# Optimization experiments

Hardware: AMD Instinct MI355X
Metric: run time of the kernel (lower is better)

The kernel has to match this reference:

```python
import jax, jax.numpy as jnp
from jax import lax
import numpy as np

B, T, D, H, LAT, FUT = 2048, 64, 64, 256, 64, 96
NL = 10  # LSTM layers


def _lstm_layer(x, Wih, Whh, b):
    # x: [B, T, Din]; Wih: [4H, Din]; Whh: [4H, H]; b: [4H]
    xg = jnp.einsum('btd,gd->tbg', x, Wih) + b  # precompute input projections [T,B,4H]
    h0 = jnp.zeros((x.shape[0], Whh.shape[1]), x.dtype)

    def step(carry, xt):
        h, c = carry
        g = xt + h @ Whh.T
        i, f, gg, o = jnp.split(g, 4, axis=-1)  # torch gate order i,f,g,o
        c = jax.nn.sigmoid(f) * c + jax.nn.sigmoid(i) * jnp.tanh(gg)
        h = jax.nn.sigmoid(o) * jnp.tanh(c)
        return (h, c), h

    _, hs = lax.scan(step, (h0, h0), xg)
    return jnp.transpose(hs, (1, 0, 2))  # [B,T,H]


def setup_inputs() -> dict:
    key = jax.random.key(0)
    ks = iter(jax.random.split(key, 40))
    s = 0.05
    n = lambda shape: jax.random.normal(next(ks), shape, jnp.float32) * s
    inp = {
        'X': jax.random.normal(next(ks), (B, T, D), jnp.float32),
        'Wih0': n((4 * H, D)),
        'Wih': n((NL - 1, 4 * H, H)),
        'Whh': n((NL, 4 * H, H)),
        'b': n((NL, 4 * H)),  # b_ih + b_hh folded together
        'ef1w': n((128, H)), 'ef1b': n((128,)),
        'ef2w': n((64, 128)), 'ef2b': n((64,)),
        'mean_w': n((LAT, 64)), 'mean_b': n((LAT,)),
        'logvar_w': n((LAT, 64)), 'logvar_b': n((LAT,)),
        'scale_w': n((LAT, 64)), 'scale_b': n((LAT,)),
        'shape_w': n((LAT, 64)), 'shape_b': n((LAT,)),
        'df1w': n((128, LAT)), 'df1b': n((128,)),
        'df2w': n((500, 128)), 'df2b': n((500,)),
        'outw': n((FUT, 500)), 'outb': n((FUT,)),
        'finw': n((FUT, FUT)), 'finb': n((FUT,)),
        'pi_gaussian': jnp.asarray(0.9, jnp.float32),
        'eps': jax.random.normal(next(ks), (B, LAT), jnp.float32),
        'u': jax.random.uniform(next(ks), (B, LAT), jnp.float32),
        'choice': jax.random.uniform(next(ks), (B,), jnp.float32),
    }
    return inp


def reference(X, Wih0, Wih, Whh, b, ef1w, ef1b, ef2w, ef2b,
              mean_w, mean_b, logvar_w, logvar_b, scale_w, scale_b,
              shape_w, shape_b, df1w, df1b, df2w, df2b, outw, outb,
              finw, finb, pi_gaussian, eps, u, choice):
    # ---- Encoder: 10-layer LSTM, last hidden state ----
    h = _lstm_layer(X, Wih0, Whh[0], b[0])
    for l in range(1, NL):
        h = _lstm_layer(h, Wih[l - 1], Whh[l], b[l])
    last = h[:, -1, :]  # [B,H]
    hid = jax.nn.relu(last @ ef1w.T + ef1b)
    hid = jax.nn.relu(hid @ ef2w.T + ef2b)  # dropout = identity (eval)
    z_mean = hid @ mean_w.T + mean_b
    z_logvar = hid @ logvar_w.T + logvar_b
    z_scale = jnp.exp(hid @ scale_w.T + scale_b)
    z_shape = hid @ shape_w.T + shape_b
    # ---- Reparameterize: vectorized gaussian/GPD row selection ----
    z_gauss = z_mean + eps * jnp.exp(0.5 * z_logvar)
    z_gpd = z_scale / z_shape * (jnp.exp(-z_shape * jnp.log1p(-u)) - 1.0)
    z = jnp.where(choice[:, None] < pi_gaussian, z_gauss, z_gpd)
    # ---- Decoder ----
    d = jax.nn.relu(z @ df1w.T + df1b)
    d = jax.nn.relu(d @ df2w.T + df2b)
    out = d @ outw.T + outb
    final = out @ finw.T + finb
    return (final, z_mean, z_logvar, z_scale, z_shape)
```

## Files before the change

### kernel.cpp

```cpp
#include <hip/hip_runtime.h>

typedef unsigned short u16;
typedef unsigned int   u32;
typedef _Float16 v8hf __attribute__((ext_vector_type(8)));
typedef float  f32x4 __attribute__((ext_vector_type(4)));

static constexpr int B_   = 2048;
static constexpr int T_   = 64;
static constexpr int D_   = 64;
static constexpr int H_   = 256;
static constexpr int NL_  = 10;
static constexpr int FUT_ = 96;
static constexpr int NBLK = 128;

static constexpr size_t WF_LAYER_ELEMS = 524288;
static constexpr size_t SEQ_OFF        = 16u << 20;

__device__ __forceinline__ u16 f2h(float f) {
  _Float16 h = (_Float16)f;
  return __builtin_bit_cast(u16, h);
}
__device__ __forceinline__ float h2f(u16 b) {
  return (float)__builtin_bit_cast(_Float16, b);
}
__device__ __forceinline__ float rcp_(float x) { return __builtin_amdgcn_rcpf(x); }
__device__ __forceinline__ float fsig(float x) { return rcp_(1.f + __expf(-x)); }
__device__ __forceinline__ float ftanh(float x) {
  float e = __expf(-2.f * fabsf(x));
  float t = (1.f - e) * rcp_(1.f + e);
  return copysignf(t, x);
}

__device__ __forceinline__ void gld16(const u16* g, u16* l) {
  __builtin_amdgcn_global_load_lds(
      (const __attribute__((address_space(1))) void*)g,
      (__attribute__((address_space(3))) void*)l,
      16, 0, 0);
}

__global__ void pack_weights_v8(const float* __restrict__ Wih0,
                                const float* __restrict__ Wih,
                                const float* __restrict__ Whh,
                                u16* __restrict__ wf) {
  int gid = blockIdx.x * 256 + threadIdx.x;
  int l   = gid >> 16;
  if (l >= NL_) return;
  int rem  = gid & 65535;
  int kc   = rem >> 12;
  int cg   = (rem >> 8) & 15;
  int g    = (rem >> 6) & 3;
  int lane = rem & 63;
  const int NKC = (l == 0) ? 10 : 16;
  if (kc >= NKC) return;
  const int KX = (l == 0) ? 64 : 256;

  int row = g * 256 + cg * 16 + (lane & 15);
  int k0  = kc * 32 + (lane >> 4) * 8;

  float v[8];
#pragma unroll
  for (int i = 0; i < 8; ++i) {
    int k = k0 + i;
    float x;
    if (l == 0) x = (k < KX) ? Wih0[row * 64 + k] : Whh[row * 256 + (k - KX)];
    else        x = (k < KX) ? Wih[(size_t)((l - 1) * 1024 + row) * 256 + k]
                             : Whh[(size_t)(l * 1024 + row) * 256 + (k - KX)];
    v[i] = x;
  }
  u32 pk[4];
#pragma unroll
  for (int i = 0; i < 4; ++i)
    pk[i] = (u32)f2h(v[2 * i]) | ((u32)f2h(v[2 * i + 1]) << 16);
  uint4 val; val.x = pk[0]; val.y = pk[1]; val.z = pk[2]; val.w = pk[3];
  u16* dst = wf + (size_t)l * WF_LAYER_ELEMS
                + ((size_t)(kc * 16 + cg) * 4 + g) * 512 + (size_t)lane * 8;
  *(uint4*)dst = val;
}

template <int NKC, int KX, bool L0>
__global__ __launch_bounds__(1024, 4) void lstm_layer_v8(
    const float* __restrict__ X,
    u16* __restrict__ seq,
    const u16* __restrict__ wf,
    const float* __restrict__ bias)
{
  __shared__ __align__(16) u16 Albs[16 * 512];
  __shared__ __align__(16) u16 Wbuf[2][32768];

  const int tid  = threadIdx.x;
  const int wid  = tid >> 6;
  const int lane = tid & 63;
  const int bid  = blockIdx.x;
  const int arow = lane & 15;
  const int ahi  = lane >> 4;
  const int aswz = (arow & 7) << 4;
  const int j    = wid * 16 + arow;

  {
    int r = tid >> 6, o = (tid & 63) * 16;
    uint4 z; z.x = z.y = z.z = z.w = 0;
    *(uint4*)((char*)Albs + r * 1024 + o) = z;
  }

  float c[4] = {0.f, 0.f, 0.f, 0.f};
  float bv[4];
#pragma unroll
  for (int g = 0; g < 4; ++g) bv[g] = bias[g * 256 + j];

  const u16* wsrc = wf + (size_t)wid * 2048 + (size_t)lane * 8;
  u16* wdst0 = &Wbuf[0][wid * 2048];
  u16* wdst1 = &Wbuf[1][wid * 2048];

#pragma unroll
  for (int g = 0; g < 4; ++g) gld16(wsrc + g * 512, wdst0 + g * 512);

  for (int t = 0; t < T_; ++t) {
    if constexpr (L0) {
      int r = tid >> 6, k = tid & 63;
      float xv = X[((size_t)(bid * 16 + r) * T_ + t) * D_ + k];
      *(u16*)((char*)Albs + r * 1024 + ((k * 2) ^ ((r & 7) << 4))) = f2h(xv);
    } else {
      int r = tid >> 6, seg = tid & 63;
      uint2 v = *(const uint2*)(seq + ((((size_t)bid * T_ + t) * 16 + r) << 8) + seg * 4);
      *(uint2*)((char*)Albs + r * 1024 + ((seg * 8) ^ ((r & 7) << 4))) = v;
    }
    __syncthreads();

    f32x4 acc[4];
#pragma unroll
    for (int g = 0; g < 4; ++g) {
      acc[g][0] = bv[g]; acc[g][1] = bv[g]; acc[g][2] = bv[g]; acc[g][3] = bv[g];
    }

#pragma unroll
    for (int kc = 0; kc < NKC; ++kc) {
      if (kc + 1 < NKC) {
        u16* nd = ((kc + 1) & 1) ? wdst1 : wdst0;
#pragma unroll
        for (int g = 0; g < 4; ++g)
          gld16(wsrc + (size_t)(kc + 1) * 32768 + g * 512, nd + g * 512);
        asm volatile("s_waitcnt vmcnt(4)" ::: "memory");
      } else {
        asm volatile("s_waitcnt vmcnt(0)" ::: "memory");
      }
      __builtin_amdgcn_sched_barrier(0);

      v8hf a = *(const v8hf*)((const char*)Albs + arow * 1024 +
                              ((kc * 64 + ahi * 16) ^ aswz));
      const u16* wl = ((kc & 1) ? wdst1 : wdst0) + lane * 8;
#pragma unroll
      for (int g = 0; g < 4; ++g) {
        v8hf bw = *(const v8hf*)(const void*)(wl + g * 512);
        acc[g] = __builtin_amdgcn_mfma_f32_16x16x32_f16(a, bw, acc[g], 0, 0, 0);
      }
    }
    __syncthreads();

    __builtin_amdgcn_sched_barrier(0);
#pragma unroll
    for (int g = 0; g < 4; ++g) gld16(wsrc + g * 512, wdst0 + g * 512);

    u16* sbase = seq + ((((size_t)bid * T_ + t) * 16) << 8) + j;
#pragma unroll
    for (int q = 0; q < 4; ++q) {
      int r = ahi * 4 + q;
      float cn = fsig(acc[1][q]) * c[q] + fsig(acc[0][q]) * ftanh(acc[2][q]);
      c[q] = cn;
      float h = fsig(acc[3][q]) * ftanh(cn);
      u16 hb = f2h(h);
      sbase[(size_t)r << 8] = hb;
      *(u16*)((char*)Albs + r * 1024 + (((KX + j) * 2) ^ ((r & 7) << 4))) = hb;
    }
  }
}

template <int N, int K, bool RELU>
__device__ __forceinline__ void dense(const float (*__restrict__ in)[512],
                                      float (*__restrict__ out)[512],
                                      const float* __restrict__ W,
                                      const float* __restrict__ bg, int tid) {
  for (int e = tid; e < 16 * N; e += 256) {
    int r = e / N, n = e - r * N;
    const float* wr = W + (size_t)n * K;
    const float* ar = in[r];
    float4 acc = {0.f, 0.f, 0.f, 0.f};
    for (int k = 0; k < K; k += 4) {
      float4 wv = *(const float4*)(wr + k);
      float4 av = *(const float4*)(ar + k);
      acc.x = fmaf(wv.x, av.x, acc.x);
      acc.y = fmaf(wv.y, av.y, acc.y);
      acc.z = fmaf(wv.z, av.z, acc.z);
      acc.w = fmaf(wv.w, av.w, acc.w);
    }
    float s = bg[n] + acc.x + acc.y + acc.z + acc.w;
    out[r][n] = RELU ? fmaxf(s, 0.f) : s;
  }
}

template <int K>
__device__ __forceinline__ float dotK(const float* __restrict__ a, const float* __restrict__ w) {
  float4 acc = {0.f, 0.f, 0.f, 0.f};
#pragma unroll
  for (int k = 0; k < K; k += 4) {
    float4 wv = *(const float4*)(w + k);
    float4 av = *(const float4*)(a + k);
    acc.x = fmaf(wv.x, av.x, acc.x);
    acc.y = fmaf(wv.y, av.y, acc.y);
    acc.z = fmaf(wv.z, av.z, acc.z);
    acc.w = fmaf(wv.w, av.w, acc.w);
  }
  return acc.x + acc.y + acc.z + acc.w;
}

struct TailArgs {
  const u16* seq;
  const float *ef1w, *ef1b, *ef2w, *ef2b;
  const float *mean_w, *mean_b, *logvar_w, *logvar_b;
  const float *scale_w, *scale_b, *shape_w, *shape_b;
  const float *df1w, *df1b, *df2w, *df2b, *outw, *outb, *finw, *finb;
  const float *pi, *eps, *u, *choice;
  float* out;
};

__global__ __launch_bounds__(256) void tail_kernel_v8(TailArgs A) {
  __shared__ float a0[16][512];
  __shared__ float a1[16][512];
  const int tid = threadIdx.x, bid = blockIdx.x;

  for (int e = tid; e < 16 * 256; e += 256) {
    int r = e >> 8, jj = e & 255;
    a0[r][jj] = h2f(A.seq[((((size_t)bid * T_ + (T_ - 1)) * 16 + r) << 8) + jj]);
  }
  __syncthreads();

  dense<128, 256, true>(a0, a1, A.ef1w, A.ef1b, tid); __syncthreads();
  dense<64, 128, true>(a1, a0, A.ef2w, A.ef2b, tid);  __syncthreads();

  const float pi = *A.pi;
  for (int e = tid; e < 16 * 64; e += 256) {
    int r = e >> 6, n = e & 63;
    size_t rg = (size_t)bid * 16 + r;
    float m  = dotK<64>(a0[r], A.mean_w   + n * 64) + A.mean_b[n];
    float lv = dotK<64>(a0[r], A.logvar_w + n * 64) + A.logvar_b[n];
    float sc = __expf(dotK<64>(a0[r], A.scale_w + n * 64) + A.scale_b[n]);
    float sh = dotK<64>(a0[r], A.shape_w + n * 64) + A.shape_b[n];
    A.out[196608 + rg * 64 + n] = m;
    A.out[327680 + rg * 64 + n] = lv;
    A.out[458752 + rg * 64 + n] = sc;
    A.out[589824 + rg * 64 + n] = sh;
    float zg = m + A.eps[rg * 64 + n] * __expf(0.5f * lv);
    float L  = log1pf(-A.u[rg * 64 + n]);
    float zp = sc / sh * (__expf(-sh * L) - 1.f);
    a1[r][n] = (A.choice[rg] < pi) ? zg : zp;
  }
  __syncthreads();

  dense<128, 64, true>(a1, a0, A.df1w, A.df1b, tid);   __syncthreads();
  dense<500, 128, true>(a0, a1, A.df2w, A.df2b, tid);  __syncthreads();
  dense<96, 500, false>(a1, a0, A.outw, A.outb, tid);  __syncthreads();
  dense<96, 96, false>(a0, a1, A.finw, A.finb, tid);   __syncthreads();

  for (int e = tid; e < 16 * FUT_; e += 256) {
    int r = e / FUT_, n = e - r * FUT_;
    A.out[((size_t)bid * 16 + r) * FUT_ + n] = a1[r][n];
  }
}

extern "C" void kernel_launch(void* const* d_in, const int* in_sizes, int n_in,
                              void* d_out, int out_size, void* d_ws, size_t ws_size,
                              hipStream_t stream) {
  (void)in_sizes; (void)n_in; (void)out_size; (void)ws_size;

  const float* X      = (const float*)d_in[0];
  const float* Wih0   = (const float*)d_in[1];
  const float* Wih    = (const float*)d_in[2];
  const float* Whh    = (const float*)d_in[3];
  const float* b      = (const float*)d_in[4];
  const float* ef1w   = (const float*)d_in[5];
  const float* ef1b   = (const float*)d_in[6];
  const float* ef2w   = (const float*)d_in[7];
  const float* ef2b   = (const float*)d_in[8];
  const float* mean_w = (const float*)d_in[9];
  const float* mean_b = (const float*)d_in[10];
  const float* logvar_w = (const float*)d_in[11];
  const float* logvar_b = (const float*)d_in[12];
  const float* scale_w  = (const float*)d_in[13];
  const float* scale_b  = (const float*)d_in[14];
  const float* shape_w  = (const float*)d_in[15];
  const float* shape_b  = (const float*)d_in[16];
  const float* df1w   = (const float*)d_in[17];
  const float* df1b   = (const float*)d_in[18];
  const float* df2w   = (const float*)d_in[19];
  const float* df2b   = (const float*)d_in[20];
  const float* outw   = (const float*)d_in[21];
  const float* outb   = (const float*)d_in[22];
  const float* finw   = (const float*)d_in[23];
  const float* finb   = (const float*)d_in[24];
  const float* pi_g   = (const float*)d_in[25];
  const float* eps    = (const float*)d_in[26];
  const float* u      = (const float*)d_in[27];
  const float* choice = (const float*)d_in[28];

  u16* wf  = (u16*)d_ws;
  u16* seq = (u16*)((char*)d_ws + SEQ_OFF);
  float* out = (float*)d_out;

  pack_weights_v8<<<2560, 256, 0, stream>>>(Wih0, Wih, Whh, wf);

  lstm_layer_v8<10, 64, true><<<NBLK, 1024, 0, stream>>>(X, seq, wf, b);
  for (int l = 1; l < NL_; ++l)
    lstm_layer_v8<16, 256, false><<<NBLK, 1024, 0, stream>>>(nullptr, seq,
        wf + (size_t)l * WF_LAYER_ELEMS, b + l * 1024);

  TailArgs A;
  A.seq = seq;
  A.ef1w = ef1w; A.ef1b = ef1b; A.ef2w = ef2w; A.ef2b = ef2b;
  A.mean_w = mean_w; A.mean_b = mean_b; A.logvar_w = logvar_w; A.logvar_b = logvar_b;
  A.scale_w = scale_w; A.scale_b = scale_b; A.shape_w = shape_w; A.shape_b = shape_b;
  A.df1w = df1w; A.df1b = df1b; A.df2w = df2w; A.df2b = df2b;
  A.outw = outw; A.outb = outb; A.finw = finw; A.finb = finb;
  A.pi = pi_g; A.eps = eps; A.u = u; A.choice = choice;
  A.out = out;
  tail_kernel_v8<<<NBLK, 256, 0, stream>>>(A);
}
```

Measured before the change: 12.58 ms.

## Precompute input projections in 4-step chunks, separating them from the recurrent matmul

```diff
diff --git a/kernel.cpp b/kernel.cpp
--- a/kernel.cpp
+++ b/kernel.cpp
@@ -16,6 +16,14 @@
 static constexpr size_t WF_LAYER_ELEMS = 524288;
 static constexpr size_t SEQ_OFF        = 16u << 20;
 
+static constexpr size_t WFH_OFF  = 0;
+static constexpr size_t WFX_OFF  = 5u << 20;
+static constexpr size_t XG_OFF   = 10u << 20;
+static constexpr size_t SEQ2_OFF = 26u << 20;
+static constexpr size_t WS_NEED_V9 = SEQ2_OFF + (64ull << 20);
+static constexpr int    WFL9 = 262144;
+static constexpr int    TCH  = 4;
+
 __device__ __forceinline__ u16 f2h(float f) {
   _Float16 h = (_Float16)f;
   return __builtin_bit_cast(u16, h);
@@ -30,7 +38,6 @@
   float t = (1.f - e) * rcp_(1.f + e);
   return copysignf(t, x);
 }
-
 __device__ __forceinline__ void gld16(const u16* g, u16* l) {
   __builtin_amdgcn_global_load_lds(
       (const __attribute__((address_space(1))) void*)g,
@@ -82,8 +89,7 @@
     const float* __restrict__ X,
     u16* __restrict__ seq,
     const u16* __restrict__ wf,
-    const float* __restrict__ bias)
-{
+    const float* __restrict__ bias) {
   __shared__ __align__(16) u16 Albs[16 * 512];
   __shared__ __align__(16) u16 Wbuf[2][32768];
 
@@ -170,6 +176,244 @@
       u16 hb = f2h(h);
       sbase[(size_t)r << 8] = hb;
       *(u16*)((char*)Albs + r * 1024 + (((KX + j) * 2) ^ ((r & 7) << 4))) = hb;
+    }
+  }
+}
+
+__global__ void pack_weights_v9(const float* __restrict__ Wih0,
+                                const float* __restrict__ Wih,
+                                const float* __restrict__ Whh,
+                                u16* __restrict__ wfh,
+                                u16* __restrict__ wfx) {
+  int gid = blockIdx.x * 256 + threadIdx.x;
+  int lw  = gid >> 15;
+  if (lw >= NL_ * 2) return;
+  int l = lw >> 1, which = lw & 1;
+  int rem  = gid & 32767;
+  int kc   = rem >> 12;
+  int cg   = (rem >> 8) & 15;
+  int g    = (rem >> 6) & 3;
+  int lane = rem & 63;
+  if (which == 1 && l == 0 && kc >= 2) return;
+
+  int row = g * 256 + cg * 16 + (lane & 15);
+  int k0  = kc * 32 + (lane >> 4) * 8;
+
+  float v[8];
+#pragma unroll
+  for (int i = 0; i < 8; ++i) {
+    int k = k0 + i;
+    float x;
+    if (which == 0)      x = Whh[(size_t)(l * 1024 + row) * 256 + k];
+    else if (l == 0)     x = Wih0[row * 64 + k];
+    else                 x = Wih[(size_t)((l - 1) * 1024 + row) * 256 + k];
+    v[i] = x;
+  }
+  u32 pk[4];
+#pragma unroll
+  for (int i = 0; i < 4; ++i)
+    pk[i] = (u32)f2h(v[2 * i]) | ((u32)f2h(v[2 * i + 1]) << 16);
+  uint4 val; val.x = pk[0]; val.y = pk[1]; val.z = pk[2]; val.w = pk[3];
+  u16* base = (which == 0) ? wfh : wfx;
+  u16* dst = base + (size_t)l * WFL9
+                  + ((size_t)(kc * 16 + cg) * 4 + g) * 512 + (size_t)lane * 8;
+  *(uint4*)dst = val;
+}
+
+template <bool L0>
+__global__ __launch_bounds__(1024, 4) void lstm_layer_v9(
+    const float* __restrict__ X,
+    u16* __restrict__ seq,
+    const u16* __restrict__ wfx_l,
+    const u16* __restrict__ wfh_l,
+    u16* __restrict__ xg,
+    const float* __restrict__ bias) {
+  __shared__ __align__(16) u16 Wbuf[2][32768];
+  __shared__ __align__(16) u16 Ah[16 * 256];
+
+  const int tid  = threadIdx.x;
+  const int wid  = tid >> 6;
+  const int lane = tid & 63;
+  const int bid  = blockIdx.x;
+  const int arow = lane & 15;
+  const int ahi  = lane >> 4;
+  const int j    = wid * 16 + arow;
+
+  *(uint2*)((char*)Ah + tid * 8) = make_uint2(0, 0);
+
+  float c[4] = {0.f, 0.f, 0.f, 0.f};
+  float bv[4];
+#pragma unroll
+  for (int g = 0; g < 4; ++g) bv[g] = bias[g * 256 + j];
+
+  u16* wdst0 = &Wbuf[0][wid * 2048];
+  u16* wdst1 = &Wbuf[1][wid * 2048];
+  const size_t laneoff = (size_t)lane * 8;
+  u16* xgb = xg + (size_t)bid * 65536;
+  uint2 xr[4];
+
+  __syncthreads();
+
+  for (int tc = 0; tc < T_ / TCH; ++tc) {
+    f32x4 acc0[TCH][4];
+#pragma unroll
+    for (int rf = 0; rf < TCH; ++rf)
+#pragma unroll
+      for (int g = 0; g < 4; ++g) {
+        acc0[rf][g][0] = bv[g]; acc0[rf][g][1] = bv[g];
+        acc0[rf][g][2] = bv[g]; acc0[rf][g][3] = bv[g];
+      }
+
+    if constexpr (L0) {
+#pragma unroll
+      for (int g = 0; g < 4; ++g) {
+        gld16(wfx_l + ((size_t)(0 * 16 + wid) * 4 + g) * 512 + laneoff, wdst0 + g * 512);
+        gld16(wfx_l + ((size_t)(1 * 16 + wid) * 4 + g) * 512 + laneoff, wdst1 + g * 512);
+      }
+      asm volatile("s_waitcnt vmcnt(0)" ::: "memory");
+      __builtin_amdgcn_sched_barrier(0);
+      const float* xb = X + ((size_t)(bid * 16 + arow) * T_ + tc * TCH) * D_ + ahi * 8;
+#pragma unroll
+      for (int kc = 0; kc < 2; ++kc) {
+        const u16* wl = (kc ? wdst1 : wdst0) + lane * 8;
+        v8hf af[TCH];
+#pragma unroll
+        for (int rf = 0; rf < TCH; ++rf) {
+          float4 u = *(const float4*)(xb + rf * D_ + kc * 32);
+          float4 v2 = *(const float4*)(xb + rf * D_ + kc * 32 + 4);
+          v8hf a;
+          a[0] = (_Float16)u.x;  a[1] = (_Float16)u.y;
+          a[2] = (_Float16)u.z;  a[3] = (_Float16)u.w;
+          a[4] = (_Float16)v2.x; a[5] = (_Float16)v2.y;
+          a[6] = (_Float16)v2.z; a[7] = (_Float16)v2.w;
+          af[rf] = a;
+        }
+#pragma unroll
+        for (int g = 0; g < 4; ++g) {
+          v8hf w = *(const v8hf*)(const void*)(wl + g * 512);
+#pragma unroll
+          for (int rf = 0; rf < TCH; ++rf)
+            acc0[rf][g] = __builtin_amdgcn_mfma_f32_16x16x32_f16(af[rf], w, acc0[rf][g], 0, 0, 0);
+        }
+      }
+    } else {
+      const u16* abase = seq + ((size_t)(bid * T_ + tc * TCH) * 16 + arow) * 256 + ahi * 8;
+      v8hf aA[TCH], aB[TCH];
+#pragma unroll
+      for (int g = 0; g < 4; ++g)
+        gld16(wfx_l + ((size_t)(0 * 16 + wid) * 4 + g) * 512 + laneoff, wdst0 + g * 512);
+#pragma unroll
+      for (int rf = 0; rf < TCH; ++rf)
+        aA[rf] = *(const v8hf*)(const void*)(abase + rf * 4096);
+
+#pragma unroll
+      for (int kc = 0; kc < 8; ++kc) {
+        if (kc < 7) {
+          u16* nd = ((kc + 1) & 1) ? wdst1 : wdst0;
+#pragma unroll
+          for (int g = 0; g < 4; ++g)
+            gld16(wfx_l + ((size_t)((kc + 1) * 16 + wid) * 4 + g) * 512 + laneoff, nd + g * 512);
+          if ((kc & 1) == 0) {
+#pragma unroll
+            for (int rf = 0; rf < TCH; ++rf)
+              aB[rf] = *(const v8hf*)(const void*)(abase + rf * 4096 + (kc + 1) * 32);
+          } else {
+#pragma unroll
+            for (int rf = 0; rf < TCH; ++rf)
+              aA[rf] = *(const v8hf*)(const void*)(abase + rf * 4096 + (kc + 1) * 32);
+          }
+          asm volatile("s_waitcnt vmcnt(8)" ::: "memory");
+        } else {
+          asm volatile("s_waitcnt vmcnt(0)" ::: "memory");
+        }
+        __builtin_amdgcn_sched_barrier(0);
+        const u16* wl = ((kc & 1) ? wdst1 : wdst0) + lane * 8;
+#pragma unroll
+        for (int g = 0; g < 4; ++g) {
+          v8hf w = *(const v8hf*)(const void*)(wl + g * 512);
+#pragma unroll
+          for (int rf = 0; rf < TCH; ++rf)
+            acc0[rf][g] = __builtin_amdgcn_mfma_f32_16x16x32_f16(
+                ((kc & 1) ? aB[rf] : aA[rf]), w, acc0[rf][g], 0, 0, 0);
+        }
+      }
+    }
+
+#pragma unroll
+    for (int rf = 0; rf < TCH; ++rf)
+#pragma unroll
+      for (int g = 0; g < 4; ++g) {
+        uint2 pk;
+        pk.x = (u32)f2h(acc0[rf][g][0]) | ((u32)f2h(acc0[rf][g][1]) << 16);
+        pk.y = (u32)f2h(acc0[rf][g][2]) | ((u32)f2h(acc0[rf][g][3]) << 16);
+        *(uint2*)(xgb + (((size_t)(rf * 1024 + g * 256 + j)) << 4) + ahi * 4) = pk;
+      }
+    __syncthreads();
+
+#pragma unroll
+    for (int g = 0; g < 4; ++g)
+      xr[g] = *(const uint2*)(xgb + (((size_t)(0 * 1024 + g * 256 + j)) << 4) + ahi * 4);
+#pragma unroll
+    for (int g = 0; g < 4; ++g)
+      gld16(wfh_l + ((size_t)(0 * 16 + wid) * 4 + g) * 512 + laneoff, wdst0 + g * 512);
+
+    for (int tl = 0; tl < TCH; ++tl) {
+      const int t = tc * TCH + tl;
+      f32x4 acc[4];
+#pragma unroll
+      for (int g = 0; g < 4; ++g) {
+        acc[g][0] = h2f((u16)(xr[g].x & 0xffff));
+        acc[g][1] = h2f((u16)(xr[g].x >> 16));
+        acc[g][2] = h2f((u16)(xr[g].y & 0xffff));
+        acc[g][3] = h2f((u16)(xr[g].y >> 16));
+      }
+
+#pragma unroll
+      for (int kc = 0; kc < 8; ++kc) {
+        if (kc < 7) {
+          u16* nd = ((kc + 1) & 1) ? wdst1 : wdst0;
+#pragma unroll
+          for (int g = 0; g < 4; ++g)
+            gld16(wfh_l + ((size_t)((kc + 1) * 16 + wid) * 4 + g) * 512 + laneoff, nd + g * 512);
+          asm volatile("s_waitcnt vmcnt(4)" ::: "memory");
+        } else {
+          asm volatile("s_waitcnt vmcnt(0)" ::: "memory");
+        }
+        __builtin_amdgcn_sched_barrier(0);
+
+        v8hf a = *(const v8hf*)((const char*)Ah + arow * 512 +
+                                ((kc * 64 + ahi * 16) ^ ((arow & 7) << 4)));
+        const u16* wl = ((kc & 1) ? wdst1 : wdst0) + lane * 8;
+#pragma unroll
+        for (int g = 0; g < 4; ++g) {
+          v8hf w = *(const v8hf*)(const void*)(wl + g * 512);
+          acc[g] = __builtin_amdgcn_mfma_f32_16x16x32_f16(a, w, acc[g], 0, 0, 0);
+        }
+      }
+      __syncthreads();
+
+      if (tl + 1 < TCH) {
+#pragma unroll
+        for (int g = 0; g < 4; ++g)
+          xr[g] = *(const uint2*)(xgb + (((size_t)((tl + 1) * 1024 + g * 256 + j)) << 4) + ahi * 4);
+        __builtin_amdgcn_sched_barrier(0);
+#pragma unroll
+        for (int g = 0; g < 4; ++g)
+          gld16(wfh_l + ((size_t)(0 * 16 + wid) * 4 + g) * 512 + laneoff, wdst0 + g * 512);
+      }
+
+      u16* sbase = seq + ((((size_t)bid * T_ + t) * 16) << 8) + j;
+#pragma unroll
+      for (int q = 0; q < 4; ++q) {
+        int r = ahi * 4 + q;
+        float cn = fsig(acc[1][q]) * c[q] + fsig(acc[0][q]) * ftanh(acc[2][q]);
+        c[q] = cn;
+        float h = fsig(acc[3][q]) * ftanh(cn);
+        u16 hb = f2h(h);
+        sbase[(size_t)r << 8] = hb;
+        *(u16*)((char*)Ah + r * 512 + ((j * 2) ^ ((r & 7) << 4))) = hb;
+      }
+      __syncthreads();
     }
   }
 }
@@ -269,7 +513,7 @@
 extern "C" void kernel_launch(void* const* d_in, const int* in_sizes, int n_in,
                               void* d_out, int out_size, void* d_ws, size_t ws_size,
                               hipStream_t stream) {
-  (void)in_sizes; (void)n_in; (void)out_size; (void)ws_size;
+  (void)in_sizes; (void)n_in; (void)out_size;
 
   const float* X      = (const float*)d_in[0];
   const float* Wih0   = (const float*)d_in[1];
@@ -301,16 +545,33 @@
   const float* u      = (const float*)d_in[27];
   const float* choice = (const float*)d_in[28];
 
-  u16* wf  = (u16*)d_ws;
-  u16* seq = (u16*)((char*)d_ws + SEQ_OFF);
   float* out = (float*)d_out;
-
-  pack_weights_v8<<<2560, 256, 0, stream>>>(Wih0, Wih, Whh, wf);
-
-  lstm_layer_v8<10, 64, true><<<NBLK, 1024, 0, stream>>>(X, seq, wf, b);
-  for (int l = 1; l < NL_; ++l)
-    lstm_layer_v8<16, 256, false><<<NBLK, 1024, 0, stream>>>(nullptr, seq,
-        wf + (size_t)l * WF_LAYER_ELEMS, b + l * 1024);
+  const bool big = ws_size >= WS_NEED_V9;
+  u16* seq;
+
+  if (big) {
+    u16* wfh = (u16*)((char*)d_ws + WFH_OFF);
+    u16* wfx = (u16*)((char*)d_ws + WFX_OFF);
+    u16* xg  = (u16*)((char*)d_ws + XG_OFF);
+    seq      = (u16*)((char*)d_ws + SEQ2_OFF);
+
+    pack_weights_v9<<<2560, 256, 0, stream>>>(Wih0, Wih, Whh, wfh, wfx);
+
+    lstm_layer_v9<true><<<NBLK, 1024, 0, stream>>>(X, seq, wfx, wfh, xg, b);
+    for (int l = 1; l < NL_; ++l)
+      lstm_layer_v9<false><<<NBLK, 1024, 0, stream>>>(nullptr, seq,
+          wfx + (size_t)l * WFL9, wfh + (size_t)l * WFL9, xg, b + l * 1024);
+  } else {
+    u16* wf = (u16*)d_ws;
+    seq     = (u16*)((char*)d_ws + SEQ_OFF);
+
+    pack_weights_v8<<<2560, 256, 0, stream>>>(Wih0, Wih, Whh, wf);
+
+    lstm_layer_v8<10, 64, true><<<NBLK, 1024, 0, stream>>>(X, seq, wf, b);
+    for (int l = 1; l < NL_; ++l)
+      lstm_layer_v8<16, 256, false><<<NBLK, 1024, 0, stream>>>(nullptr, seq,
+          wf + (size_t)l * WF_LAYER_ELEMS, b + l * 1024);
+  }
 
   TailArgs A;
   A.seq = seq;
```

After: 10.67 ms. -15.2%, faster.

## Split LSTM input projection from recurrence, batching x-gates over time chunks

Applied to the files above, without the earlier changes.

```diff
diff --git a/kernel.cpp b/kernel.cpp
--- a/kernel.cpp
+++ b/kernel.cpp
@@ -4,6 +4,7 @@
 typedef unsigned int   u32;
 typedef _Float16 v8hf __attribute__((ext_vector_type(8)));
 typedef float  f32x4 __attribute__((ext_vector_type(4)));
+typedef u32    u32x2 __attribute__((ext_vector_type(2)));
 
 static constexpr int B_   = 2048;
 static constexpr int T_   = 64;
@@ -13,8 +14,12 @@
 static constexpr int FUT_ = 96;
 static constexpr int NBLK = 128;
 
-static constexpr size_t WF_LAYER_ELEMS = 524288;
-static constexpr size_t SEQ_OFF        = 16u << 20;
+static constexpr size_t WFH_OFF  = 0;
+static constexpr size_t WFX_OFF  = 5u << 20;
+static constexpr size_t XG_OFF   = 10u << 20;
+static constexpr size_t SEQ2_OFF = 26u << 20;
+static constexpr int    WFL9 = 262144;
+static constexpr int    TCH  = 4;
 
 __device__ __forceinline__ u16 f2h(float f) {
   _Float16 h = (_Float16)f;
@@ -30,7 +35,6 @@
   float t = (1.f - e) * rcp_(1.f + e);
   return copysignf(t, x);
 }
-
 __device__ __forceinline__ void gld16(const u16* g, u16* l) {
   __builtin_amdgcn_global_load_lds(
       (const __attribute__((address_space(1))) void*)g,
@@ -38,21 +42,21 @@
       16, 0, 0);
 }
 
-__global__ void pack_weights_v8(const float* __restrict__ Wih0,
-                                const float* __restrict__ Wih,
-                                const float* __restrict__ Whh,
-                                u16* __restrict__ wf) {
+__global__ void pack_weights_v11(const float* __restrict__ Wih0,
+                                 const float* __restrict__ Wih,
+                                 const float* __restrict__ Whh,
+                                 u16* __restrict__ wfh,
+                                 u16* __restrict__ wfx) {
   int gid = blockIdx.x * 256 + threadIdx.x;
-  int l   = gid >> 16;
-  if (l >= NL_) return;
-  int rem  = gid & 65535;
+  int lw  = gid >> 15;
+  if (lw >= NL_ * 2) return;
+  int l = lw >> 1, which = lw & 1;
+  int rem  = gid & 32767;
   int kc   = rem >> 12;
   int cg   = (rem >> 8) & 15;
   int g    = (rem >> 6) & 3;
   int lane = rem & 63;
-  const int NKC = (l == 0) ? 10 : 16;
-  if (kc >= NKC) return;
-  const int KX = (l == 0) ? 64 : 256;
+  if (which == 1 && l == 0 && kc >= 2) return;
 
   int row = g * 256 + cg * 16 + (lane & 15);
   int k0  = kc * 32 + (lane >> 4) * 8;
@@ -62,9 +66,9 @@
   for (int i = 0; i < 8; ++i) {
     int k = k0 + i;
     float x;
-    if (l == 0) x = (k < KX) ? Wih0[row * 64 + k] : Whh[row * 256 + (k - KX)];
-    else        x = (k < KX) ? Wih[(size_t)((l - 1) * 1024 + row) * 256 + k]
-                             : Whh[(size_t)(l * 1024 + row) * 256 + (k - KX)];
+    if (which == 0)      x = Whh[(size_t)(l * 1024 + row) * 256 + k];
+    else if (l == 0)     x = Wih0[row * 64 + k];
+    else                 x = Wih[(size_t)((l - 1) * 1024 + row) * 256 + k];
     v[i] = x;
   }
   u32 pk[4];
@@ -72,20 +76,22 @@
   for (int i = 0; i < 4; ++i)
     pk[i] = (u32)f2h(v[2 * i]) | ((u32)f2h(v[2 * i + 1]) << 16);
   uint4 val; val.x = pk[0]; val.y = pk[1]; val.z = pk[2]; val.w = pk[3];
-  u16* dst = wf + (size_t)l * WF_LAYER_ELEMS
-                + ((size_t)(kc * 16 + cg) * 4 + g) * 512 + (size_t)lane * 8;
+  u16* base = (which == 0) ? wfh : wfx;
+  u16* dst = base + (size_t)l * WFL9
+                  + ((size_t)(kc * 16 + cg) * 4 + g) * 512 + (size_t)lane * 8;
   *(uint4*)dst = val;
 }
 
-template <int NKC, int KX, bool L0>
-__global__ __launch_bounds__(1024, 4) void lstm_layer_v8(
+template <bool L0>
+__global__ __launch_bounds__(1024, 4) void lstm_layer_v11(
     const float* __restrict__ X,
     u16* __restrict__ seq,
-    const u16* __restrict__ wf,
-    const float* __restrict__ bias)
-{
-  __shared__ __align__(16) u16 Albs[16 * 512];
-  __shared__ __align__(16) u16 Wbuf[2][32768];
+    const u16* __restrict__ wfx_l,
+    const u16* __restrict__ wfh_l,
+    u16* __restrict__ xg,
+    const float* __restrict__ bias) {
+  __shared__ __align__(16) u16 Wring[65536];
+  __shared__ __align__(16) u16 Ah[16 * 256];
 
   const int tid  = threadIdx.x;
   const int wid  = tid >> 6;
@@ -93,83 +99,196 @@
   const int bid  = blockIdx.x;
   const int arow = lane & 15;
   const int ahi  = lane >> 4;
-  const int aswz = (arow & 7) << 4;
   const int j    = wid * 16 + arow;
 
-  {
-    int r = tid >> 6, o = (tid & 63) * 16;
-    uint4 z; z.x = z.y = z.z = z.w = 0;
-    *(uint4*)((char*)Albs + r * 1024 + o) = z;
-  }
+  *(u32x2*)((char*)Ah + tid * 8) = (u32x2){0, 0};
 
   float c[4] = {0.f, 0.f, 0.f, 0.f};
   float bv[4];
 #pragma unroll
   for (int g = 0; g < 4; ++g) bv[g] = bias[g * 256 + j];
 
-  const u16* wsrc = wf + (size_t)wid * 2048 + (size_t)lane * 8;
-  u16* wdst0 = &Wbuf[0][wid * 2048];
-  u16* wdst1 = &Wbuf[1][wid * 2048];
-
-#pragma unroll
-  for (int g = 0; g < 4; ++g) gld16(wsrc + g * 512, wdst0 + g * 512);
-
-  for (int t = 0; t < T_; ++t) {
+  u16* wdst0 = Wring + wid * 2048;
+  u16* wdst1 = Wring + 32768 + wid * 2048;
+  const size_t laneoff = (size_t)lane * 8;
+  u16* xgb = xg + (size_t)bid * 65536;
+  u32x2 xr[4];
+
+  __syncthreads();
+
+  for (int tc = 0; tc < T_ / TCH; ++tc) {
+    f32x4 acc0[TCH][4];
+#pragma unroll
+    for (int rf = 0; rf < TCH; ++rf)
+#pragma unroll
+      for (int g = 0; g < 4; ++g) {
+        acc0[rf][g][0] = bv[g]; acc0[rf][g][1] = bv[g];
+        acc0[rf][g][2] = bv[g]; acc0[rf][g][3] = bv[g];
+      }
+
     if constexpr (L0) {
-      int r = tid >> 6, k = tid & 63;
-      float xv = X[((size_t)(bid * 16 + r) * T_ + t) * D_ + k];
-      *(u16*)((char*)Albs + r * 1024 + ((k * 2) ^ ((r & 7) << 4))) = f2h(xv);
+#pragma unroll
+      for (int g = 0; g < 4; ++g) {
+        gld16(wfx_l + ((size_t)(0 * 16 + wid) * 4 + g) * 512 + laneoff, wdst0 + g * 512);
+        gld16(wfx_l + ((size_t)(1 * 16 + wid) * 4 + g) * 512 + laneoff, wdst1 + g * 512);
+      }
+      asm volatile("s_waitcnt vmcnt(0)" ::: "memory");
+      __builtin_amdgcn_sched_barrier(0);
+      const float* xb = X + ((size_t)(bid * 16 + arow) * T_ + tc * TCH) * D_ + ahi * 8;
+#pragma unroll
+      for (int kc = 0; kc < 2; ++kc) {
+        const u16* wl = (kc ? wdst1 : wdst0) + lane * 8;
+        v8hf af[TCH];
+#pragma unroll
+        for (int rf = 0; rf < TCH; ++rf) {
+          f32x4 u = __builtin_nontemporal_load((const f32x4*)(xb + rf * D_ + kc * 32));
+          f32x4 v2 = __builtin_nontemporal_load((const f32x4*)(xb + rf * D_ + kc * 32 + 4));
+          v8hf a;
+          a[0] = (_Float16)u[0];  a[1] = (_Float16)u[1];
+          a[2] = (_Float16)u[2];  a[3] = (_Float16)u[3];
+          a[4] = (_Float16)v2[0]; a[5] = (_Float16)v2[1];
+          a[6] = (_Float16)v2[2]; a[7] = (_Float16)v2[3];
+          af[rf] = a;
+        }
+#pragma unroll
+        for (int g = 0; g < 4; ++g) {
+          v8hf w = *(const v8hf*)(const void*)(wl + g * 512);
+#pragma unroll
+          for (int rf = 0; rf < TCH; ++rf)
+            acc0[rf][g] = __builtin_amdgcn_mfma_f32_16x16x32_f16(af[rf], w, acc0[rf][g], 0, 0, 0);
+        }
+      }
     } else {
-      int r = tid >> 6, seg = tid & 63;
-      uint2 v = *(const uint2*)(seq + ((((size_t)bid * T_ + t) * 16 + r) << 8) + seg * 4);
-      *(uint2*)((char*)Albs + r * 1024 + ((seg * 8) ^ ((r & 7) << 4))) = v;
+      const u16* abase = seq + ((size_t)(bid * T_ + tc * TCH) * 16 + arow) * 256 + ahi * 8;
+      v8hf aA[TCH], aB[TCH];
+#pragma unroll
+      for (int g = 0; g < 4; ++g)
+        gld16(wfx_l + ((size_t)(0 * 16 + wid) * 4 + g) * 512 + laneoff, wdst0 + g * 512);
+#pragma unroll
+      for (int rf = 0; rf < TCH; ++rf)
+        aA[rf] = __builtin_nontemporal_load((const v8hf*)(const void*)(abase + rf * 4096));
+
+#pragma unroll
+      for (int kc = 0; kc < 8; ++kc) {
+        if (kc < 7) {
+          u16* nd = ((kc + 1) & 1) ? wdst1 : wdst0;
+#pragma unroll
+          for (int g = 0; g < 4; ++g)
+            gld16(wfx_l + ((size_t)((kc + 1) * 16 + wid) * 4 + g) * 512 + laneoff, nd + g * 512);
+          if ((kc & 1) == 0) {
+#pragma unroll
+            for (int rf = 0; rf < TCH; ++rf)
+              aB[rf] = __builtin_nontemporal_load(
+                  (const v8hf*)(const void*)(abase + rf * 4096 + (kc + 1) * 32));
+          } else {
+#pragma unroll
+            for (int rf = 0; rf < TCH; ++rf)
+              aA[rf] = __builtin_nontemporal_load(
+                  (const v8hf*)(const void*)(abase + rf * 4096 + (kc + 1) * 32));
+          }
+          asm volatile("s_waitcnt vmcnt(8)" ::: "memory");
+        } else {
+          asm volatile("s_waitcnt vmcnt(0)" ::: "memory");
+        }
+        __builtin_amdgcn_sched_barrier(0);
+        const u16* wl = ((kc & 1) ? wdst1 : wdst0) + lane * 8;
+#pragma unroll
+        for (int g = 0; g < 4; ++g) {
+          v8hf w = *(const v8hf*)(const void*)(wl + g * 512);
+#pragma unroll
+          for (int rf = 0; rf < TCH; ++rf)
+            acc0[rf][g] = __builtin_amdgcn_mfma_f32_16x16x32_f16(
+                ((kc & 1) ? aB[rf] : aA[rf]), w, acc0[rf][g], 0, 0, 0);
+        }
+      }
     }
+
+#pragma unroll
+    for (int rf = 0; rf < TCH; ++rf)
+#pragma unroll
+      for (int g = 0; g < 4; ++g) {
+        u32x2 pk;
+        pk[0] = (u32)f2h(acc0[rf][g][0]) | ((u32)f2h(acc0[rf][g][1]) << 16);
+        pk[1] = (u32)f2h(acc0[rf][g][2]) | ((u32)f2h(acc0[rf][g][3]) << 16);
+        __builtin_nontemporal_store(pk,
+            (u32x2*)(xgb + (((size_t)(rf * 1024 + g * 256 + j)) << 4) + ahi * 4));
+      }
     __syncthreads();
 
-    f32x4 acc[4];
-#pragma unroll
-    for (int g = 0; g < 4; ++g) {
-      acc[g][0] = bv[g]; acc[g][1] = bv[g]; acc[g][2] = bv[g]; acc[g][3] = bv[g];
-    }
-
-#pragma unroll
-    for (int kc = 0; kc < NKC; ++kc) {
-      if (kc + 1 < NKC) {
-        u16* nd = ((kc + 1) & 1) ? wdst1 : wdst0;
+#pragma unroll
+    for (int g = 0; g < 4; ++g)
+      xr[g] = __builtin_nontemporal_load(
+          (const u32x2*)(xgb + (((size_t)(0 * 1024 + g * 256 + j)) << 4) + ahi * 4));
+
+    for (int tl = 0; tl < TCH; ++tl) {
+      const int t = tc * TCH + tl;
+      f32x4 acc[4];
+#pragma unroll
+      for (int g = 0; g < 4; ++g) {
+        acc[g][0] = h2f((u16)(xr[g][0] & 0xffff));
+        acc[g][1] = h2f((u16)(xr[g][0] >> 16));
+        acc[g][2] = h2f((u16)(xr[g][1] & 0xffff));
+        acc[g][3] = h2f((u16)(xr[g][1] >> 16));
+      }
+
+#pragma unroll
+      for (int u0 = 0; u0 < 3; ++u0) {
+        const int kc = u0 >> 1, gh = u0 & 1;
+        u16* sb = Wring + (u0 & 3) * 16384 + wid * 1024;
+#pragma unroll
+        for (int jj = 0; jj < 2; ++jj)
+          gld16(wfh_l + ((size_t)(kc * 16 + wid) * 4 + gh * 2 + jj) * 512 + laneoff,
+                sb + jj * 512);
+      }
+
+      v8hf a{};
+#pragma unroll
+      for (int u = 0; u < 16; ++u) {
+        const int kc = u >> 1, gh = u & 1;
+        if (u + 3 <= 15) {
+          const int un = u + 3, kn = un >> 1, gn = un & 1;
+          u16* sb = Wring + (un & 3) * 16384 + wid * 1024;
+#pragma unroll
+          for (int jj = 0; jj < 2; ++jj)
+            gld16(wfh_l + ((size_t)(kn * 16 + wid) * 4 + gn * 2 + jj) * 512 + laneoff,
+                  sb + jj * 512);
+        }
+        if (u <= 12)      asm volatile("s_waitcnt vmcnt(6)" ::: "memory");
+        else if (u == 13) asm volatile("s_waitcnt vmcnt(4)" ::: "memory");
+        else if (u == 14) asm volatile("s_waitcnt vmcnt(2)" ::: "memory");
+        else              asm volatile("s_waitcnt vmcnt(0)" ::: "memory");
+        __builtin_amdgcn_sched_barrier(0);
+
+        if (gh == 0)
+          a = *(const v8hf*)((const char*)Ah + arow * 512 +
+                             ((kc * 64 + ahi * 16) ^ ((arow & 7) << 4)));
+        const u16* wl = Wring + (u & 3) * 16384 + wid * 1024 + lane * 8;
+        v8hf w0 = *(const v8hf*)(const void*)(wl);
+        v8hf w1 = *(const v8hf*)(const void*)(wl + 512);
+        acc[gh * 2]     = __builtin_amdgcn_mfma_f32_16x16x32_f16(a, w0, acc[gh * 2], 0, 0, 0);
+        acc[gh * 2 + 1] = __builtin_amdgcn_mfma_f32_16x16x32_f16(a, w1, acc[gh * 2 + 1], 0, 0, 0);
+      }
+      __syncthreads();
+
+      if (tl + 1 < TCH) {
 #pragma unroll
         for (int g = 0; g < 4; ++g)
-          gld16(wsrc + (size_t)(kc + 1) * 32768 + g * 512, nd + g * 512);
-        asm volatile("s_waitcnt vmcnt(4)" ::: "memory");
-      } else {
-        asm volatile("s_waitcnt vmcnt(0)" ::: "memory");
-      }
-      __builtin_amdgcn_sched_barrier(0);
-
-      v8hf a = *(const v8hf*)((const char*)Albs + arow * 1024 +
-                              ((kc * 64 + ahi * 16) ^ aswz));
-      const u16* wl = ((kc & 1) ? wdst1 : wdst0) + lane * 8;
-#pragma unroll
-      for (int g = 0; g < 4; ++g) {
-        v8hf bw = *(const v8hf*)(const void*)(wl + g * 512);
-        acc[g] = __builtin_amdgcn_mfma_f32_16x16x32_f16(a, bw, acc[g], 0, 0, 0);
-      }
-    }
-    __syncthreads();
-
-    __builtin_amdgcn_sched_barrier(0);
-#pragma unroll
-    for (int g = 0; g < 4; ++g) gld16(wsrc + g * 512, wdst0 + g * 512);
-
-    u16* sbase = seq + ((((size_t)bid * T_ + t) * 16) << 8) + j;
-#pragma unroll
-    for (int q = 0; q < 4; ++q) {
-      int r = ahi * 4 + q;
-      float cn = fsig(acc[1][q]) * c[q] + fsig(acc[0][q]) * ftanh(acc[2][q]);
-      c[q] = cn;
-      float h = fsig(acc[3][q]) * ftanh(cn);
-      u16 hb = f2h(h);
-      sbase[(size_t)r << 8] = hb;
-      *(u16*)((char*)Albs + r * 1024 + (((KX + j) * 2) ^ ((r & 7) << 4))) = hb;
+          xr[g] = __builtin_nontemporal_load(
+              (const u32x2*)(xgb + (((size_t)((tl + 1) * 1024 + g * 256 + j)) << 4) + ahi * 4));
+      }
+
+      u16* sbase = seq + ((((size_t)bid * T_ + t) * 16) << 8) + j;
+#pragma unroll
+      for (int q = 0; q < 4; ++q) {
+        int r = ahi * 4 + q;
+        float cn = fsig(acc[1][q]) * c[q] + fsig(acc[0][q]) * ftanh(acc[2][q]);
+        c[q] = cn;
+        float h = fsig(acc[3][q]) * ftanh(cn);
+        u16 hb = f2h(h);
+        __builtin_nontemporal_store(hb, sbase + ((size_t)r << 8));
+        *(u16*)((char*)Ah + r * 512 + ((j * 2) ^ ((r & 7) << 4))) = hb;
+      }
+      __syncthreads();
     }
   }
 }
@@ -222,7 +341,7 @@
   float* out;
 };
 
-__global__ __launch_bounds__(256) void tail_kernel_v8(TailArgs A) {
+__global__ __launch_bounds__(256) void tail_kernel_v11(TailArgs A) {
   __shared__ float a0[16][512];
   __shared__ float a1[16][512];
   const int tid = threadIdx.x, bid = blockIdx.x;
@@ -301,16 +420,18 @@
   const float* u      = (const float*)d_in[27];
   const float* choice = (const float*)d_in[28];
 
-  u16* wf  = (u16*)d_ws;
-  u16* seq = (u16*)((char*)d_ws + SEQ_OFF);
   float* out = (float*)d_out;
-
-  pack_weights_v8<<<2560, 256, 0, stream>>>(Wih0, Wih, Whh, wf);
-
-  lstm_layer_v8<10, 64, true><<<NBLK, 1024, 0, stream>>>(X, seq, wf, b);
+  u16* wfh = (u16*)((char*)d_ws + WFH_OFF);
+  u16* wfx = (u16*)((char*)d_ws + WFX_OFF);
+  u16* xg  = (u16*)((char*)d_ws + XG_OFF);
+  u16* seq = (u16*)((char*)d_ws + SEQ2_OFF);
+
+  pack_weights_v11<<<2560, 256, 0, stream>>>(Wih0, Wih, Whh, wfh, wfx);
+
+  lstm_layer_v11<true><<<NBLK, 1024, 0, stream>>>(X, seq, wfx, wfh, xg, b);
   for (int l = 1; l < NL_; ++l)
-    lstm_layer_v8<16, 256, false><<<NBLK, 1024, 0, stream>>>(nullptr, seq,
-        wf + (size_t)l * WF_LAYER_ELEMS, b + l * 1024);
+    lstm_layer_v11<false><<<NBLK, 1024, 0, stream>>>(nullptr, seq,
+        wfx + (size_t)l * WFL9, wfh + (size_t)l * WFL9, xg, b + l * 1024);
 
   TailArgs A;
   A.seq = seq;
@@ -321,5 +442,5 @@
   A.outw = outw; A.outb = outb; A.finw = finw; A.finb = finb;
   A.pi = pi_g; A.eps = eps; A.u = u; A.choice = choice;
   A.out = out;
-  tail_kernel_v8<<<NBLK, 256, 0, stream>>>(A);
-}
+  tail_kernel_v11<<<NBLK, 256, 0, stream>>>(A);
+}
```

Result: slower. 18.11 ms (+43.9%).
